# Optimization experiments

Hardware: AMD Instinct MI355X
Metric: run time of the kernel (lower is better)

## Reference

```python
import jax, jax.numpy as jnp
import numpy as np

B, F, D = 1024, 16, 64
P = F * (F - 1) // 2  # 120 field pairs


def setup_inputs() -> dict:
    key = jax.random.key(0)
    k1, k2, k3 = jax.random.split(key, 3)
    x = jax.random.normal(k1, (B, F, D), dtype=jnp.float32)
    # torch Linear weight layout: [out_features, in_features] = [D, D*D], one per pair
    W = jax.random.normal(k2, (P, D, D * D), dtype=jnp.float32) * (1.0 / np.sqrt(D * D))
    b = jax.random.normal(k3, (P, D), dtype=jnp.float32) * 0.01
    return {"x": x, "W": W, "b": b}


def reference(x, W, b):
    # x: [B, F, D]; W: [P, D, D*D]; b: [P, D]
    Bs, Fs, Ds = x.shape
    Ps = W.shape[0]
    ii, jj = np.triu_indices(Fs, k=1)  # pair order matches nested (i, j>i) loop
    xi = x[:, ii, :]  # [B, P, D] -> left vector of outer product
    xj = x[:, jj, :]  # [B, P, D] -> right vector
    # Flattened outer tmp[b, a*D + c] = xi[b,p,a] * xj[b,p,c];
    # Linear: out = tmp @ W^T + b. Reshape W to [P, D_out, a, c] and fuse,
    # never materializing the [B, P, D*D] outer-product tensor.
    W3 = W.reshape(Ps, Ds, Ds, Ds)
    out = jnp.einsum('bpa,bpc,pkac->bpk', xi, xj, W3) + b[None, :, :]
    return out  # [B, P, D]
```

## Files before the change

### kernel.cpp

```cpp
#include <hip/hip_runtime.h>
#include <stdint.h>
#include <stddef.h>

constexpr int NB = 1024;
constexpr int NF = 16;
constexpr int ND = 64;
constexpr int NP = 120;
constexpr int KD = ND * ND;
constexpr int OUT_STRIDE = NP * ND;

constexpr int BM = 256;

using floatx4 = __attribute__((ext_vector_type(4))) float;
using half8   = __attribute__((ext_vector_type(8))) _Float16;
using half2v  = __attribute__((ext_vector_type(2))) _Float16;
using fp16x2  = __attribute__((ext_vector_type(2))) __fp16;
using uint4v  = __attribute__((ext_vector_type(4))) uint32_t;

constexpr int XT_STRIDE = BM;
constexpr int BT_STRIDE = ND;
constexpr int BT_BUF    = ND * BT_STRIDE;

__device__ __forceinline__ half2v pkh2(float f0, float f1) {
    fp16x2 h = __builtin_amdgcn_cvt_pkrtz(f0, f1);
    return __builtin_bit_cast(half2v, h);
}
__device__ __forceinline__ uint32_t pk16(float f0, float f1) {
    fp16x2 h = __builtin_amdgcn_cvt_pkrtz(f0, f1);
    return __builtin_bit_cast(uint32_t, h);
}
__device__ __forceinline__ uint16_t f16bits(float f) {
    return __builtin_bit_cast(uint16_t, (_Float16)f);
}

__global__ __launch_bounds__(512, 4)
void outer_kernel(const float* __restrict__ x, const float* __restrict__ W,
                  const float* __restrict__ bias, float* __restrict__ out)
{
    __shared__ uint16_t lds_xit[ND * XT_STRIDE];
    __shared__ uint16_t lds_bt[2 * BT_BUF];

    const int p  = blockIdx.x;
    const int b0 = blockIdx.y * BM;

    int icol = 0, rem = p;
    while (rem >= NF - 1 - icol) { rem -= NF - 1 - icol; ++icol; }
    const int jcol = icol + 1 + rem;

    const int t    = threadIdx.x;
    const int wave = t >> 6;
    const int lane = t & 63;
    const int r    = lane & 15;
    const int quad = lane >> 4;

    {
        const int mrow  = t >> 1;
        const int chalf = (t & 1) * 32;
        const float* src = x + (size_t)(b0 + mrow) * (NF * ND) + icol * ND + chalf;
        #pragma unroll
        for (int c = 0; c < 32; c += 4) {
            floatx4 v = *(const floatx4*)(src + c);
            lds_xit[(chalf + c + 0) * XT_STRIDE + mrow] = f16bits(v.x);
            lds_xit[(chalf + c + 1) * XT_STRIDE + mrow] = f16bits(v.y);
            lds_xit[(chalf + c + 2) * XT_STRIDE + mrow] = f16bits(v.z);
            lds_xit[(chalf + c + 3) * XT_STRIDE + mrow] = f16bits(v.w);
        }
    }

    half2v xjh[2][8];
    #pragma unroll
    for (int ms = 0; ms < 2; ++ms) {
        const float* srow = x + (size_t)(b0 + wave*32 + ms*16 + r) * (NF * ND)
                              + jcol * ND + quad * 8;
        #pragma unroll
        for (int ks = 0; ks < 2; ++ks) {
            floatx4 v0 = *(const floatx4*)(srow + ks * 32);
            floatx4 v1 = *(const floatx4*)(srow + ks * 32 + 4);
            xjh[ms][ks*4 + 0] = pkh2(v0.x, v0.y);
            xjh[ms][ks*4 + 1] = pkh2(v0.z, v0.w);
            xjh[ms][ks*4 + 2] = pkh2(v1.x, v1.y);
            xjh[ms][ks*4 + 3] = pkh2(v1.z, v1.w);
        }
    }

    const int n_st = t >> 3;
    const int cg   = t & 7;
    const float* wsrc = W + ((size_t)p * ND + n_st) * KD + cg * 8;
    uint16_t* bdst0 = &lds_bt[n_st * BT_STRIDE + ((cg ^ (n_st & 7)) * 8)];

    floatx4 wreg[2];

    wreg[0] = *(const floatx4*)(wsrc);
    wreg[1] = *(const floatx4*)(wsrc + 4);
    {
        uint4v q0 = (uint4v){ pk16(wreg[0].x, wreg[0].y), pk16(wreg[0].z, wreg[0].w),
                              pk16(wreg[1].x, wreg[1].y), pk16(wreg[1].z, wreg[1].w) };
        *(uint4v*)(bdst0) = q0;
    }
    wreg[0] = *(const floatx4*)(wsrc + ND);
    wreg[1] = *(const floatx4*)(wsrc + ND + 4);
    __syncthreads();

    floatx4 acc[2][4] = {};

    const int xg0 = (quad ^ (r & 7)) * 8;

    #pragma unroll 1
    for (int a = 0; a < ND; ++a) {
        const int cur = a & 1;
        const uint16_t* rbuf = lds_bt + cur * BT_BUF;

        uint32_t xiu[2];
        #pragma unroll
        for (int ms = 0; ms < 2; ++ms)
            xiu[ms] = lds_xit[a * XT_STRIDE + wave*32 + ms*16 + r];

        half8 bfr[4][2];
        #pragma unroll
        for (int ns = 0; ns < 4; ++ns) {
            const int rowb = (ns*16 + r) * BT_STRIDE;
            bfr[ns][0] = *(const half8*)&rbuf[rowb + xg0];
            bfr[ns][1] = *(const half8*)&rbuf[rowb + (xg0 ^ 32)];
        }

        half8 pa0[2], pa1[2];
        #pragma unroll
        for (int ms = 0; ms < 2; ++ms) {
            half2v xs = __builtin_bit_cast(half2v,
                __builtin_amdgcn_perm(xiu[ms], xiu[ms], 0x01000100u));
            union { half8 h8; half2v h2[4]; } u0, u1;
            #pragma unroll
            for (int q2 = 0; q2 < 4; ++q2) {
                u0.h2[q2] = xs * xjh[ms][q2];
                u1.h2[q2] = xs * xjh[ms][4 + q2];
            }
            pa0[ms] = u0.h8;
            pa1[ms] = u1.h8;
        }

        #pragma unroll
        for (int ns = 0; ns < 4; ++ns) {
            #pragma unroll
            for (int ms = 0; ms < 2; ++ms) {
                acc[ms][ns] = __builtin_amdgcn_mfma_f32_16x16x32_f16(
                    pa0[ms], bfr[ns][0], acc[ms][ns], 0, 0, 0);
                acc[ms][ns] = __builtin_amdgcn_mfma_f32_16x16x32_f16(
                    pa1[ms], bfr[ns][1], acc[ms][ns], 0, 0, 0);
            }
        }

        if (a + 1 < ND) {
            uint16_t* bd = bdst0 + (cur ^ 1) * BT_BUF;
            uint4v q0 = (uint4v){ pk16(wreg[0].x, wreg[0].y), pk16(wreg[0].z, wreg[0].w),
                                  pk16(wreg[1].x, wreg[1].y), pk16(wreg[1].z, wreg[1].w) };
            *(uint4v*)(bd) = q0;
        }
        if (a + 2 < ND) {
            const float* wn = wsrc + (size_t)(a + 2) * ND;
            wreg[0] = *(const floatx4*)(wn);
            wreg[1] = *(const floatx4*)(wn + 4);
        }

        __syncthreads();
    }

    #pragma unroll
    for (int ns = 0; ns < 4; ++ns) {
        const float bb = bias[p * ND + ns*16 + r];
        #pragma unroll
        for (int ms = 0; ms < 2; ++ms) {
            #pragma unroll
            for (int reg = 0; reg < 4; ++reg) {
                const int row = b0 + wave*32 + ms*16 + quad*4 + reg;
                out[(size_t)row * OUT_STRIDE + p * ND + ns*16 + r]
                    = acc[ms][ns][reg] + bb;
            }
        }
    }
}

extern "C" void kernel_launch(void* const* d_in, const int* in_sizes, int n_in,
                              void* d_out, int out_size, void* d_ws, size_t ws_size,
                              hipStream_t stream) {
    const float* x    = (const float*)d_in[0];
    const float* W    = (const float*)d_in[1];
    const float* bias = (const float*)d_in[2];
    float* out = (float*)d_out;

    dim3 grid(NP, NB / BM);
    outer_kernel<<<grid, 512, 0, stream>>>(x, W, bias, out);
}
```

Measured before the change: 219.0 us.

## Retile waves as 4x2 grid so each wave covers 64 rows by 32 outputs

Each of the 8 waves now computes a 64-row by 32-column output tile instead of 32 rows by all 64 columns. The xi transpose in shared memory is permuted so a wave reads its four row-slices' xi values with one 8-byte load per step. The aim is to halve per-wave B-fragment LDS reads and reuse each B fragment across four M-subtiles. In exchange, each wave builds twice as many outer-product A fragments on the VALU and holds more xj registers.

Result: no change. 223.3 us (+2.0%).

```diff
diff --git a/kernel.cpp b/kernel.cpp
--- a/kernel.cpp
+++ b/kernel.cpp
@@ -16,8 +16,8 @@
 using half2v  = __attribute__((ext_vector_type(2))) _Float16;
 using fp16x2  = __attribute__((ext_vector_type(2))) __fp16;
 using uint4v  = __attribute__((ext_vector_type(4))) uint32_t;
+using ushort4v = __attribute__((ext_vector_type(4))) uint16_t;
 
-constexpr int XT_STRIDE = BM;
 constexpr int BT_STRIDE = ND;
 constexpr int BT_BUF    = ND * BT_STRIDE;
 
@@ -37,7 +37,7 @@
 void outer_kernel(const float* __restrict__ x, const float* __restrict__ W,
                   const float* __restrict__ bias, float* __restrict__ out)
 {
-    __shared__ uint16_t lds_xit[ND * XT_STRIDE];
+    __shared__ uint16_t lds_xit[ND * BM];
     __shared__ uint16_t lds_bt[2 * BT_BUF];
 
     const int p  = blockIdx.x;
@@ -52,25 +52,29 @@
     const int lane = t & 63;
     const int r    = lane & 15;
     const int quad = lane >> 4;
+    const int wm   = wave & 3;
+    const int wn   = wave >> 2;
 
     {
         const int mrow  = t >> 1;
         const int chalf = (t & 1) * 32;
+        const int wms = mrow >> 6, mss = (mrow >> 4) & 3, rs = mrow & 15;
+        const int dbase = wms * 64 + rs * 4 + mss;
         const float* src = x + (size_t)(b0 + mrow) * (NF * ND) + icol * ND + chalf;
         #pragma unroll
         for (int c = 0; c < 32; c += 4) {
             floatx4 v = *(const floatx4*)(src + c);
-            lds_xit[(chalf + c + 0) * XT_STRIDE + mrow] = f16bits(v.x);
-            lds_xit[(chalf + c + 1) * XT_STRIDE + mrow] = f16bits(v.y);
-            lds_xit[(chalf + c + 2) * XT_STRIDE + mrow] = f16bits(v.z);
-            lds_xit[(chalf + c + 3) * XT_STRIDE + mrow] = f16bits(v.w);
+            lds_xit[(chalf + c + 0) * BM + dbase] = f16bits(v.x);
+            lds_xit[(chalf + c + 1) * BM + dbase] = f16bits(v.y);
+            lds_xit[(chalf + c + 2) * BM + dbase] = f16bits(v.z);
+            lds_xit[(chalf + c + 3) * BM + dbase] = f16bits(v.w);
         }
     }
 
-    half2v xjh[2][8];
+    half2v xjh[4][8];
     #pragma unroll
-    for (int ms = 0; ms < 2; ++ms) {
-        const float* srow = x + (size_t)(b0 + wave*32 + ms*16 + r) * (NF * ND)
+    for (int ms = 0; ms < 4; ++ms) {
+        const float* srow = x + (size_t)(b0 + wm*64 + ms*16 + r) * (NF * ND)
                               + jcol * ND + quad * 8;
         #pragma unroll
         for (int ks = 0; ks < 2; ++ks) {
@@ -101,7 +105,7 @@
     wreg[1] = *(const floatx4*)(wsrc + ND + 4);
     __syncthreads();
 
-    floatx4 acc[2][4] = {};
+    floatx4 acc[4][2] = {};
 
     const int xg0 = (quad ^ (r & 7)) * 8;
 
@@ -110,42 +114,34 @@
         const int cur = a & 1;
         const uint16_t* rbuf = lds_bt + cur * BT_BUF;
 
-        uint32_t xiu[2];
+        union { ushort4v s4; uint32_t u[2]; } xiu;
+        xiu.s4 = *(const ushort4v*)&lds_xit[a * BM + wm * 64 + r * 4];
+
+        half8 bfr[2][2];
         #pragma unroll
-        for (int ms = 0; ms < 2; ++ms)
-            xiu[ms] = lds_xit[a * XT_STRIDE + wave*32 + ms*16 + r];
-
-        half8 bfr[4][2];
-        #pragma unroll
-        for (int ns = 0; ns < 4; ++ns) {
-            const int rowb = (ns*16 + r) * BT_STRIDE;
+        for (int ns = 0; ns < 2; ++ns) {
+            const int rowb = (wn*32 + ns*16 + r) * BT_STRIDE;
             bfr[ns][0] = *(const half8*)&rbuf[rowb + xg0];
             bfr[ns][1] = *(const half8*)&rbuf[rowb + (xg0 ^ 32)];
         }
 
-        half8 pa0[2], pa1[2];
         #pragma unroll
-        for (int ms = 0; ms < 2; ++ms) {
-            half2v xs = __builtin_bit_cast(half2v,
-                __builtin_amdgcn_perm(xiu[ms], xiu[ms], 0x01000100u));
+        for (int ms = 0; ms < 4; ++ms) {
+            const uint32_t xw = xiu.u[ms >> 1];
+            const uint32_t sel = (ms & 1) ? 0x03020302u : 0x01000100u;
+            half2v xs = __builtin_bit_cast(half2v, __builtin_amdgcn_perm(xw, xw, sel));
             union { half8 h8; half2v h2[4]; } u0, u1;
             #pragma unroll
             for (int q2 = 0; q2 < 4; ++q2) {
                 u0.h2[q2] = xs * xjh[ms][q2];
                 u1.h2[q2] = xs * xjh[ms][4 + q2];
             }
-            pa0[ms] = u0.h8;
-            pa1[ms] = u1.h8;
-        }
-
-        #pragma unroll
-        for (int ns = 0; ns < 4; ++ns) {
             #pragma unroll
-            for (int ms = 0; ms < 2; ++ms) {
+            for (int ns = 0; ns < 2; ++ns) {
                 acc[ms][ns] = __builtin_amdgcn_mfma_f32_16x16x32_f16(
-                    pa0[ms], bfr[ns][0], acc[ms][ns], 0, 0, 0);
+                    u0.h8, bfr[ns][0], acc[ms][ns], 0, 0, 0);
                 acc[ms][ns] = __builtin_amdgcn_mfma_f32_16x16x32_f16(
-                    pa1[ms], bfr[ns][1], acc[ms][ns], 0, 0, 0);
+                    u1.h8, bfr[ns][1], acc[ms][ns], 0, 0, 0);
             }
         }
 
@@ -156,23 +152,23 @@
             *(uint4v*)(bd) = q0;
         }
         if (a + 2 < ND) {
-            const float* wn = wsrc + (size_t)(a + 2) * ND;
-            wreg[0] = *(const floatx4*)(wn);
-            wreg[1] = *(const floatx4*)(wn + 4);
+            const float* wn2 = wsrc + (size_t)(a + 2) * ND;
+            wreg[0] = *(const floatx4*)(wn2);
+            wreg[1] = *(const floatx4*)(wn2 + 4);
         }
 
         __syncthreads();
     }
 
     #pragma unroll
-    for (int ns = 0; ns < 4; ++ns) {
-        const float bb = bias[p * ND + ns*16 + r];
+    for (int ns = 0; ns < 2; ++ns) {
+        const float bb = bias[p * ND + wn*32 + ns*16 + r];
         #pragma unroll
-        for (int ms = 0; ms < 2; ++ms) {
+        for (int ms = 0; ms < 4; ++ms) {
             #pragma unroll
             for (int reg = 0; reg < 4; ++reg) {
-                const int row = b0 + wave*32 + ms*16 + quad*4 + reg;
-                out[(size_t)row * OUT_STRIDE + p * ND + ns*16 + r]
+                const int row = b0 + wm*64 + ms*16 + quad*4 + reg;
+                out[(size_t)row * OUT_STRIDE + p * ND + wn*32 + ns*16 + r]
                     = acc[ms][ns][reg] + bb;
             }
         }
```
